# Kernel optimization log

Measured on AMD Instinct MI355X. Metric: run time of the kernel, lower is better.

The kernel has to match this reference:

```python
import jax, jax.numpy as jnp
import numpy as np

B, L, E, H = 8, 1024, 512, 8
E2 = 2 * E
EPS = 1e-5


def _spectral_fc(x, w, fw, fb, n):
    # rfft along feature dim, multiply by rfft of learned filter w (1,n), irfft back, then Linear
    xf = jnp.fft.rfft(x, axis=2, norm='ortho')          # [B,L,n//2+1] complex
    wf = jnp.fft.rfft(w, axis=1, norm='ortho')          # [1,n//2+1] complex
    y = jnp.fft.irfft(xf * wf, n=n, axis=2, norm='ortho')
    return y @ fw + fb


def _layernorm(x, g, b):
    m = jnp.mean(x, axis=-1, keepdims=True)
    v = jnp.mean(jnp.square(x - m), axis=-1, keepdims=True)
    return (x - m) * jax.lax.rsqrt(v + EPS) * g + b


def setup_inputs() -> dict:
    key = jax.random.key(0)
    ks = jax.random.split(key, 32)
    s = 0.02

    def lin_w(k, i, o):
        return (jax.random.normal(k, (i, o), jnp.float32) / np.sqrt(i)).astype(jnp.float32)

    def layer_params(k0, k1, n):
        return (s * jax.random.normal(k0, (1, n), jnp.float32), lin_w(k1, n, n), jnp.zeros((n,), jnp.float32))

    attn_w, attn_fw, attn_fb = layer_params(ks[1], ks[2], E)
    ln0_w, ln0_fw, ln0_fb = layer_params(ks[3], ks[4], E)
    ln1_w, ln1_fw, ln1_fb = layer_params(ks[5], ks[6], E)
    ln2_w, ln2_fw, ln2_fb = layer_params(ks[7], ks[8], E)
    ln3_w, ln3_fw, ln3_fb = layer_params(ks[9], ks[10], E2)
    ln4_w, ln4_fw, ln4_fb = layer_params(ks[11], ks[12], E2)

    return {
        'x': jax.random.normal(ks[0], (B, L, E), jnp.float32),
        'attn_w': attn_w, 'attn_fw': attn_fw, 'attn_fb': attn_fb,
        'ln0_w': ln0_w, 'ln0_fw': ln0_fw, 'ln0_fb': ln0_fb,
        'ln1_w': ln1_w, 'ln1_fw': ln1_fw, 'ln1_fb': ln1_fb,
        'ln2_w': ln2_w, 'ln2_fw': ln2_fw, 'ln2_fb': ln2_fb,
        'ln3_w': ln3_w, 'ln3_fw': ln3_fw, 'ln3_fb': ln3_fb,
        'ln4_w': ln4_w, 'ln4_fw': ln4_fw, 'ln4_fb': ln4_fb,
        'n1_g': jnp.ones((E,), jnp.float32), 'n1_b': jnp.zeros((E,), jnp.float32),
        'n2_g': jnp.ones((E,), jnp.float32), 'n2_b': jnp.zeros((E,), jnp.float32),
    }


def reference(x, attn_w, attn_fw, attn_fb,
              ln0_w, ln0_fw, ln0_fb, ln1_w, ln1_fw, ln1_fb,
              ln2_w, ln2_fw, ln2_fb, ln3_w, ln3_fw, ln3_fb,
              ln4_w, ln4_fw, ln4_fb, n1_g, n1_b, n2_g, n2_b):
    q = _spectral_fc(x, attn_w, attn_fw, attn_fb, E).reshape(B, L, H, E // H)
    scores = jnp.einsum('blhe,bshe->bhls', q, q) * (1.0 / np.sqrt(E))
    A = jax.nn.softmax(scores, axis=-1)
    new_x = jnp.einsum('bhls,bshd->blhd', A, q).reshape(B, L, E)

    x1 = _layernorm(x + new_x, n1_g, n1_b)
    x_ln = jax.nn.gelu(_spectral_fc(x1, ln0_w, ln0_fw, ln0_fb, E), approximate=False)
    x2 = x1 - x_ln
    h = jax.nn.sigmoid(_spectral_fc(x2, ln1_w, ln1_fw, ln1_fb, E)) * _spectral_fc(x2, ln2_w, ln2_fw, ln2_fb, E)
    out = jnp.concatenate((new_x, x_ln), axis=-1)  # [B,L,2E]
    out = jax.nn.sigmoid(_spectral_fc(out, ln3_w, ln3_fw, ln3_fb, E2)) * _spectral_fc(out, ln4_w, ln4_fw, ln4_fb, E2)
    return (_layernorm(h, n2_g, n2_b), out)
```

## Files before the change

### kernel.cpp

```cpp
#include <hip/hip_runtime.h>
#include <hip/hip_bf16.h>
#include <math.h>

typedef __hip_bfloat16 bf16;
typedef unsigned short u16;
typedef __attribute__((ext_vector_type(8))) short short8;
typedef __attribute__((ext_vector_type(4))) float f32x4;

#define NB      8
#define SEQ     1024
#define EDIM    512
#define E2DIM   1024
#define ROWS    8192
#define INV_SQRT_E 0.04419417382415922f
#define ATT_SCL    0.06375985678148161f

__device__ inline u16 f2bu(float f) {
    union { float f; unsigned u; } c; c.f = f;
    return (u16)((c.u + 0x7FFF + ((c.u >> 16) & 1)) >> 16);
}

__device__ __forceinline__ unsigned cvtpk_bf16(float lo, float hi) {
    unsigned r;
    asm("v_cvt_pk_bf16_f32 %0, %1, %2" : "=v"(r) : "v"(lo), "v"(hi));
    return r;
}

#define VMCNT(N) do { \
    asm volatile("s_waitcnt vmcnt(" #N ")" ::: "memory"); \
    __builtin_amdgcn_sched_barrier(0); \
    __builtin_amdgcn_s_barrier(); \
    __builtin_amdgcn_sched_barrier(0); } while (0)

#define LGKM0_BAR() do { \
    asm volatile("s_waitcnt lgkmcnt(0)" ::: "memory"); \
    __builtin_amdgcn_sched_barrier(0); \
    __builtin_amdgcn_s_barrier(); \
    __builtin_amdgcn_sched_barrier(0); } while (0)

__global__ __launch_bounds__(256) void detect_dtype(const u16* __restrict__ x,
                                                    int* __restrict__ flag) {
    int t = threadIdx.x;
    int cnt = 0;
    for (int k = t; k < 8192; k += 256) {
        int e = (x[k] >> 7) & 0xFF;
        if (e >= 0xC0) cnt++;
    }
#pragma unroll
    for (int o = 32; o > 0; o >>= 1) cnt += __shfl_xor(cnt, o);
    __shared__ int red[4];
    if ((t & 63) == 0) red[t >> 6] = cnt;
    __syncthreads();
    if (t == 0) flag[0] = (red[0] + red[1] + red[2] + red[3] > 100) ? 1 : 0;
}

struct CvtBatch {
    const void* src[23];
    float4*     dst[23];
    int         pre4[24];
};

__global__ __launch_bounds__(256) void cvt_all(CvtBatch a, int total4,
                                               const int* __restrict__ flag) {
    int t = blockIdx.x * 256 + threadIdx.x;
    if (t >= total4) return;
    int lo = 0;
    while (t >= a.pre4[lo + 1]) lo++;
    int li = t - a.pre4[lo];
    if (flag[0]) {
        a.dst[lo][li] = ((const float4*)a.src[lo])[li];
    } else {
        ushort4 u = ((const ushort4*)a.src[lo])[li];
        union { unsigned int i; float f; } c;
        float4 o;
        c.i = ((unsigned)u.x) << 16; o.x = c.f;
        c.i = ((unsigned)u.y) << 16; o.y = c.f;
        c.i = ((unsigned)u.z) << 16; o.z = c.f;
        c.i = ((unsigned)u.w) << 16; o.w = c.f;
        a.dst[lo][li] = o;
    }
}

__global__ __launch_bounds__(256) void f2b_kernel(const float* __restrict__ src,
                                                  u16* __restrict__ dst, int n4) {
    int i = blockIdx.x * 256 + threadIdx.x;
    if (i >= n4) return;
    float4 a = ((const float4*)src)[i];
    ushort4 o;
    o.x = f2bu(a.x); o.y = f2bu(a.y); o.z = f2bu(a.z); o.w = f2bu(a.w);
    ((ushort4*)dst)[i] = o;
}

#define LDK 32

__device__ __forceinline__ void stage128x32(const u16* g, int ld, u16* lds, int tid) {
    const int w = tid >> 6;
    const int l = tid & 63;
    const int r = w * 16 + (l >> 2);
    const int c = (l & 3) * 8;
    const u16* g0 = g + (size_t)r * ld + c;
    u16* l0 = lds + w * 16 * LDK;
    __builtin_amdgcn_global_load_lds(
        (const __attribute__((address_space(1))) void*)g0,
        (__attribute__((address_space(3))) void*)l0, 16, 0, 0);
    const u16* g1 = g0 + (size_t)64 * ld;
    u16* l1 = l0 + 64 * LDK;
    __builtin_amdgcn_global_load_lds(
        (const __attribute__((address_space(1))) void*)g1,
        (__attribute__((address_space(3))) void*)l1, 16, 0, 0);
}

__device__ __forceinline__ void stage64x32(const u16* g, int ld, u16* lds, int tid) {
    const int w = tid >> 6;
    const int l = tid & 63;
    const int r = w * 16 + (l >> 2);
    const int c = (l & 3) * 8;
    const u16* g0 = g + (size_t)r * ld + c;
    u16* l0 = lds + w * 16 * LDK;
    __builtin_amdgcn_global_load_lds(
        (const __attribute__((address_space(1))) void*)g0,
        (__attribute__((address_space(3))) void*)l0, 16, 0, 0);
}

__device__ __forceinline__ void xcd_swz(int& bx, int& by) {
    const int nx  = gridDim.x;
    const int nwg = nx * gridDim.y;
    const int lid = blockIdx.y * nx + blockIdx.x;
    const int q   = nwg >> 3;
    const int s   = (lid & 7) * q + (lid >> 3);
    bx = s % nx;
    by = s / nx;
}

struct FoldBatch {
    const float* w[6];
    const float* fw[6];
    u16* t1[6];
    u16* t2[6];
    u16* mt[6];
    int  n[6], lg[6];
    float sc[6];
};

__global__ __launch_bounds__(256) void fold_trconv(FoldBatch fb) {
    const int z = blockIdx.z;
    const int n = fb.n[z];
    const int bx = blockIdx.x * 32, by = blockIdx.y * 32;
    if (bx >= n || by >= n) return;
    __shared__ float t[32][33];
    const int tx = threadIdx.x & 31, ty = threadIdx.x >> 5;
    const float* src = fb.fw[z];
    u16* dst = fb.t1[z];
#pragma unroll
    for (int r = 0; r < 32; r += 8)
        t[ty + r][tx] = src[(size_t)(by + ty + r) * n + bx + tx];
    __syncthreads();
#pragma unroll
    for (int r = 0; r < 32; r += 8)
        dst[(size_t)(bx + ty + r) * n + by + tx] = f2bu(t[tx][ty + r]);
}

__global__ __launch_bounds__(256) void fold_circ(FoldBatch fb) {
    const int z = blockIdx.z;
    const int n = fb.n[z], lg = fb.lg[z];
    int idx = blockIdx.x * 256 + threadIdx.x;
    if (idx >= n * n) return;
    int mask = n - 1;
    int m = idx & mask;
    int j = idx >> lg;
    fb.t2[z][idx] = f2bu(fb.w[z][(m - j) & mask]);
}

__global__ __launch_bounds__(256) void fold_gemm(FoldBatch fb) {
    const int z = blockIdx.z;
    const int n = fb.n[z];
    const int bm = blockIdx.y * 128, bn = blockIdx.x * 128;
    if (bm >= n || bn >= n) return;
    const u16* A  = fb.t1[z];
    const u16* Bt = fb.t2[z];
    u16* Mt = fb.mt[z];
    const float scale = fb.sc[z];

    __shared__ u16 Asl[2][128 * LDK];
    __shared__ u16 Bsl[2][128 * LDK];
    const int tid = threadIdx.x;
    const int lane = tid & 63, wave = tid >> 6;
    const int wy = wave >> 1, wx = wave & 1;
    const int qd = lane >> 4, ln16 = lane & 15;

    f32x4 acc[4][4];
#pragma unroll
    for (int i = 0; i < 4; i++)
#pragma unroll
        for (int j = 0; j < 4; j++)
#pragma unroll
            for (int r = 0; r < 4; r++) acc[i][j][r] = 0.f;

    const u16* Ab = A  + (size_t)bm * n;
    const u16* Bb = Bt + (size_t)bn * n;
    const int nt = n >> 5;
    stage128x32(Ab, n, Asl[0], tid);
    stage128x32(Bb, n, Bsl[0], tid);
    stage128x32(Ab + 32, n, Asl[1], tid);
    stage128x32(Bb + 32, n, Bsl[1], tid);
    int cur = 0;
    for (int t = 0; t < nt - 1; ++t) {
        VMCNT(4);
        const u16* Ac = Asl[cur];
        const u16* Bc = Bsl[cur];
        short8 af[4], bf_[4];
#pragma unroll
        for (int i = 0; i < 4; i++) {
            af[i]  = *(const short8*)&Ac[(wy * 64 + i * 16 + ln16) * LDK + qd * 8];
            bf_[i] = *(const short8*)&Bc[(wx * 64 + i * 16 + ln16) * LDK + qd * 8];
        }
        LGKM0_BAR();
        if (t + 2 < nt) {
            const int k2 = (t + 2) * 32;
            stage128x32(Ab + k2, n, Asl[cur], tid);
            stage128x32(Bb + k2, n, Bsl[cur], tid);
        }
#pragma unroll
        for (int i = 0; i < 4; i++)
#pragma unroll
            for (int j = 0; j < 4; j++)
                acc[i][j] = __builtin_amdgcn_mfma_f32_16x16x32_bf16(af[i], bf_[j], acc[i][j], 0, 0, 0);
        cur ^= 1;
    }
    VMCNT(0);
    {
        const u16* Ac = Asl[cur];
        const u16* Bc = Bsl[cur];
        short8 af[4], bf_[4];
#pragma unroll
        for (int i = 0; i < 4; i++) {
            af[i]  = *(const short8*)&Ac[(wy * 64 + i * 16 + ln16) * LDK + qd * 8];
            bf_[i] = *(const short8*)&Bc[(wx * 64 + i * 16 + ln16) * LDK + qd * 8];
        }
#pragma unroll
        for (int i = 0; i < 4; i++)
#pragma unroll
            for (int j = 0; j < 4; j++)
                acc[i][j] = __builtin_amdgcn_mfma_f32_16x16x32_bf16(af[i], bf_[j], acc[i][j], 0, 0, 0);
    }
#pragma unroll
    for (int i = 0; i < 4; i++)
#pragma unroll
        for (int j = 0; j < 4; j++) {
            const int col = bn + wx * 64 + j * 16 + ln16;
#pragma unroll
            for (int r = 0; r < 4; r++) {
                const int row = bm + wy * 64 + i * 16 + qd * 4 + r;
                Mt[(size_t)row * n + col] = f2bu(acc[i][j][r] * scale);
            }
        }
}

__global__ __launch_bounds__(256) void gemm_bf(
    const u16* __restrict__ A, int lda,
    const u16* __restrict__ Bt, int ldb,
    const float* __restrict__ bias,
    float* __restrict__ Cf, int ldc,
    u16* __restrict__ Cb, int ldcb,
    u16* __restrict__ Cb2, int ldcb2,
    const float* __restrict__ aux, int ldaux,
    int K, int mode)
{
    __shared__ u16 Asl[2][128 * LDK];
    __shared__ u16 Bsl[2][64 * LDK];
    const int tid = threadIdx.x;
    int bxs, bys;
    xcd_swz(bxs, bys);
    const int bm = bys * 128, bn = bxs * 64;
    const int lane = tid & 63, wave = tid >> 6;
    const int wy = wave >> 1, wx = wave & 1;
    const int qd = lane >> 4, ln16 = lane & 15;

    f32x4 acc[4][2];
#pragma unroll
    for (int i = 0; i < 4; i++)
#pragma unroll
        for (int j = 0; j < 2; j++)
#pragma unroll
            for (int r = 0; r < 4; r++) acc[i][j][r] = 0.f;

    const u16* Ab = A  + (size_t)bm * lda;
    const u16* Bb = Bt + (size_t)bn * ldb;
    const int nt = K >> 5;
    stage128x32(Ab, lda, Asl[0], tid);
    stage64x32(Bb, ldb, Bsl[0], tid);
    stage128x32(Ab + 32, lda, Asl[1], tid);
    stage64x32(Bb + 32, ldb, Bsl[1], tid);
    int cur = 0;
    for (int t = 0; t < nt - 1; ++t) {
        VMCNT(3);
        const u16* Ac = Asl[cur];
        const u16* Bc = Bsl[cur];
        short8 af[4], bf_[2];
#pragma unroll
        for (int i = 0; i < 4; i++)
            af[i]  = *(const short8*)&Ac[(wy * 64 + i * 16 + ln16) * LDK + qd * 8];
#pragma unroll
        for (int j = 0; j < 2; j++)
            bf_[j] = *(const short8*)&Bc[(wx * 32 + j * 16 + ln16) * LDK + qd * 8];
        LGKM0_BAR();
        if (t + 2 < nt) {
            const int k2 = (t + 2) * 32;
            stage128x32(Ab + k2, lda, Asl[cur], tid);
            stage64x32(Bb + k2, ldb, Bsl[cur], tid);
        }
#pragma unroll
        for (int i = 0; i < 4; i++)
#pragma unroll
            for (int j = 0; j < 2; j++)
                acc[i][j] = __builtin_amdgcn_mfma_f32_16x16x32_bf16(af[i], bf_[j], acc[i][j], 0, 0, 0);
        cur ^= 1;
    }
    VMCNT(0);
    {
        const u16* Ac = Asl[cur];
        const u16* Bc = Bsl[cur];
        short8 af[4], bf_[2];
#pragma unroll
        for (int i = 0; i < 4; i++)
            af[i]  = *(const short8*)&Ac[(wy * 64 + i * 16 + ln16) * LDK + qd * 8];
#pragma unroll
        for (int j = 0; j < 2; j++)
            bf_[j] = *(const short8*)&Bc[(wx * 32 + j * 16 + ln16) * LDK + qd * 8];
#pragma unroll
        for (int i = 0; i < 4; i++)
#pragma unroll
            for (int j = 0; j < 2; j++)
                acc[i][j] = __builtin_amdgcn_mfma_f32_16x16x32_bf16(af[i], bf_[j], acc[i][j], 0, 0, 0);
    }

#pragma unroll
    for (int i = 0; i < 4; i++) {
#pragma unroll
        for (int j = 0; j < 2; j++) {
            const int col = bn + wx * 32 + j * 16 + ln16;
            const float b_ = bias ? bias[col] : 0.f;
#pragma unroll
            for (int r = 0; r < 4; r++) {
                const int row = bm + wy * 64 + i * 16 + qd * 4 + r;
                float v = acc[i][j][r] + b_;
                if (mode == 1) v = 0.5f * v * (1.0f + erff(v * 0.7071067811865476f));
                if (Cf)  Cf[(size_t)row * ldc + col] = v;
                if (Cb)  Cb[(size_t)row * ldcb + col] = f2bu(v);
                if (Cb2) Cb2[(size_t)row * ldcb2 + col] =
                             f2bu(aux[(size_t)row * ldaux + col] - v);
            }
        }
    }
}

__global__ __launch_bounds__(256) void gemm_bf2(
    const u16* __restrict__ A, int lda,
    const u16* __restrict__ B1t, const u16* __restrict__ B2t, int ldb,
    const float* __restrict__ bias1, const float* __restrict__ bias2,
    float* __restrict__ Cf, int ldc, int K)
{
    __shared__ u16 Asl[2][128 * LDK];
    __shared__ u16 B1sl[2][64 * LDK];
    __shared__ u16 B2sl[2][64 * LDK];
    const int tid = threadIdx.x;
    int bxs, bys;
    xcd_swz(bxs, bys);
    const int bm = bys * 128, bn = bxs * 64;
    const int lane = tid & 63, wave = tid >> 6;
    const int wy = wave >> 1, wx = wave & 1;
    const int qd = lane >> 4, ln16 = lane & 15;

    f32x4 acc1[4][2], acc2[4][2];
#pragma unroll
    for (int i = 0; i < 4; i++)
#pragma unroll
        for (int j = 0; j < 2; j++)
#pragma unroll
            for (int r = 0; r < 4; r++) { acc1[i][j][r] = 0.f; acc2[i][j][r] = 0.f; }

    const u16* Ab  = A   + (size_t)bm * lda;
    const u16* B1b = B1t + (size_t)bn * ldb;
    const u16* B2b = B2t + (size_t)bn * ldb;
    const int nt = K >> 5;
    stage128x32(Ab,  lda, Asl[0],  tid);
    stage64x32(B1b, ldb, B1sl[0], tid);
    stage64x32(B2b, ldb, B2sl[0], tid);
    stage128x32(Ab + 32,  lda, Asl[1],  tid);
    stage64x32(B1b + 32, ldb, B1sl[1], tid);
    stage64x32(B2b + 32, ldb, B2sl[1], tid);
    int cur = 0;
    for (int t = 0; t < nt - 1; ++t) {
        VMCNT(4);
        const u16* Ac  = Asl[cur];
        const u16* B1c = B1sl[cur];
        const u16* B2c = B2sl[cur];
        short8 af[4], b1f[2], b2f[2];
#pragma unroll
        for (int i = 0; i < 4; i++)
            af[i]  = *(const short8*)&Ac [(wy * 64 + i * 16 + ln16) * LDK + qd * 8];
#pragma unroll
        for (int j = 0; j < 2; j++) {
            b1f[j] = *(const short8*)&B1c[(wx * 32 + j * 16 + ln16) * LDK + qd * 8];
            b2f[j] = *(const short8*)&B2c[(wx * 32 + j * 16 + ln16) * LDK + qd * 8];
        }
        LGKM0_BAR();
        if (t + 2 < nt) {
            const int k2 = (t + 2) * 32;
            stage128x32(Ab  + k2, lda, Asl[cur],  tid);
            stage64x32(B1b + k2, ldb, B1sl[cur], tid);
            stage64x32(B2b + k2, ldb, B2sl[cur], tid);
        }
#pragma unroll
        for (int i = 0; i < 4; i++)
#pragma unroll
            for (int j = 0; j < 2; j++) {
                acc1[i][j] = __builtin_amdgcn_mfma_f32_16x16x32_bf16(af[i], b1f[j], acc1[i][j], 0, 0, 0);
                acc2[i][j] = __builtin_amdgcn_mfma_f32_16x16x32_bf16(af[i], b2f[j], acc2[i][j], 0, 0, 0);
            }
        cur ^= 1;
    }
    VMCNT(0);
    {
        const u16* Ac  = Asl[cur];
        const u16* B1c = B1sl[cur];
        const u16* B2c = B2sl[cur];
        short8 af[4], b1f[2], b2f[2];
#pragma unroll
        for (int i = 0; i < 4; i++)
            af[i]  = *(const short8*)&Ac [(wy * 64 + i * 16 + ln16) * LDK + qd * 8];
#pragma unroll
        for (int j = 0; j < 2; j++) {
            b1f[j] = *(const short8*)&B1c[(wx * 32 + j * 16 + ln16) * LDK + qd * 8];
            b2f[j] = *(const short8*)&B2c[(wx * 32 + j * 16 + ln16) * LDK + qd * 8];
        }
#pragma unroll
        for (int i = 0; i < 4; i++)
#pragma unroll
            for (int j = 0; j < 2; j++) {
                acc1[i][j] = __builtin_amdgcn_mfma_f32_16x16x32_bf16(af[i], b1f[j], acc1[i][j], 0, 0, 0);
                acc2[i][j] = __builtin_amdgcn_mfma_f32_16x16x32_bf16(af[i], b2f[j], acc2[i][j], 0, 0, 0);
            }
    }

#pragma unroll
    for (int i = 0; i < 4; i++) {
#pragma unroll
        for (int j = 0; j < 2; j++) {
            const int col = bn + wx * 32 + j * 16 + ln16;
            const float b1_ = bias1[col], b2_ = bias2[col];
#pragma unroll
            for (int r = 0; r < 4; r++) {
                const int row = bm + wy * 64 + i * 16 + qd * 4 + r;
                const float g = 1.0f / (1.0f + expf(-(acc1[i][j][r] + b1_)));
                Cf[(size_t)row * ldc + col] = g * (acc2[i][j][r] + b2_);
            }
        }
    }
}

__global__ __launch_bounds__(256) void ln_kernel(
    const float* __restrict__ in0, int ld0,
    const u16* __restrict__ in1b, int ld1b,
    const float* __restrict__ g, const float* __restrict__ bta,
    float* __restrict__ outf, int ldo,
    u16* __restrict__ outb, int ldob)
{
    int row = blockIdx.x, tid = threadIdx.x;
    const float* p0 = in0 + (size_t)row * ld0;
    float v0 = p0[tid], v1 = p0[tid + 256];
    if (in1b) {
        const u16* p1 = in1b + (size_t)row * ld1b;
        union { unsigned u; float f; } c0, c1;
        c0.u = ((unsigned)p1[tid]) << 16;
        c1.u = ((unsigned)p1[tid + 256]) << 16;
        v0 += c0.f; v1 += c1.f;
    }
    float s = v0 + v1, sq = v0 * v0 + v1 * v1;
#pragma unroll
    for (int o = 32; o > 0; o >>= 1) {
        s  += __shfl_xor(s, o);
        sq += __shfl_xor(sq, o);
    }
    __shared__ float red[8];
    int wid = tid >> 6;
    if ((tid & 63) == 0) { red[wid] = s; red[4 + wid] = sq; }
    __syncthreads();
    s  = red[0] + red[1] + red[2] + red[3];
    sq = red[4] + red[5] + red[6] + red[7];
    float mean = s * (1.0f / 512.0f);
    float var  = sq * (1.0f / 512.0f) - mean * mean;
    float rstd = rsqrtf(var + 1e-5f);
    float o0 = (v0 - mean) * rstd * g[tid] + bta[tid];
    float o1 = (v1 - mean) * rstd * g[tid + 256] + bta[tid + 256];
    if (outf) {
        outf[(size_t)row * ldo + tid]       = o0;
        outf[(size_t)row * ldo + tid + 256] = o1;
    }
    if (outb) {
        outb[(size_t)row * ldob + tid]       = f2bu(o0);
        outb[(size_t)row * ldob + tid + 256] = f2bu(o1);
    }
}

#define AP 80

__global__ __launch_bounds__(256) void attn_mfma(const u16* __restrict__ qall,
                                                 u16* __restrict__ catb) {
    __shared__ u16 Ks[64 * AP];
    __shared__ u16 KsT[64 * AP];
    __shared__ u16 Pw[4][16 * AP];

    const int bid = blockIdx.x;
    const int lt = bid & 15, hh = (bid >> 4) & 7, bb = bid >> 7;
    const int q0 = lt * 64;
    const int tid = threadIdx.x;
    const int wave = tid >> 6, lane = tid & 63;
    const int quad = lane >> 4, ln16 = lane & 15;

    const u16* qh = qall + (size_t)bb * SEQ * EDIM + hh * 64;

    const u16* qrow = qh + (size_t)(q0 + wave * 16 + ln16) * EDIM + quad * 8;
    const short8 aq0 = *(const short8*)(qrow);
    const short8 aq1 = *(const short8*)(qrow + 32);

    f32x4 oacc[4];
    float m_run = -1e30f, l_run = 0.f;
#pragma unroll
    for (int j = 0; j < 4; j++)
#pragma unroll
        for (int r = 0; r < 4; r++) oacc[j][r] = 0.f;

    const int sr  = tid & 63;
    const int scq = (tid >> 6) * 16;

    for (int s0 = 0; s0 < SEQ; s0 += 64) {
        __syncthreads();
        {
            const u16* krow = qh + (size_t)(s0 + sr) * EDIM + scq;
            uint4 v0 = *(const uint4*)(krow);
            uint4 v1 = *(const uint4*)(krow + 8);
            *(uint4*)&Ks[sr * AP + scq]     = v0;
            *(uint4*)&Ks[sr * AP + scq + 8] = v1;
            const u16* h0 = (const u16*)&v0;
            const u16* h1 = (const u16*)&v1;
#pragma unroll
            for (int i = 0; i < 8; i++) KsT[(scq + i) * AP + sr]     = h0[i];
#pragma unroll
            for (int i = 0; i < 8; i++) KsT[(scq + 8 + i) * AP + sr] = h1[i];
        }
        __syncthreads();

        f32x4 S[4];
#pragma unroll
        for (int j = 0; j < 4; j++) {
            const int krw = (j * 16 + ln16) * AP + quad * 8;
            short8 a0 = *(const short8*)&Ks[krw];
            short8 a1 = *(const short8*)&Ks[krw + 32];
            f32x4 c = {0.f, 0.f, 0.f, 0.f};
            c = __builtin_amdgcn_mfma_f32_16x16x32_bf16(a0, aq0, c, 0, 0, 0);
            c = __builtin_amdgcn_mfma_f32_16x16x32_bf16(a1, aq1, c, 0, 0, 0);
            S[j] = c;
        }

        float mx = S[0][0];
#pragma unroll
        for (int j = 0; j < 4; j++)
#pragma unroll
            for (int r = 0; r < 4; r++) mx = fmaxf(mx, S[j][r]);
        mx = fmaxf(mx, __shfl_xor(mx, 16));
        mx = fmaxf(mx, __shfl_xor(mx, 32));
        const float mn = fmaxf(m_run, mx);
        const float al = exp2f((m_run - mn) * ATT_SCL);
        m_run = mn;
        const float ns = -mn * ATT_SCL;
        float p[4][4];
        float rs = 0.f;
#pragma unroll
        for (int j = 0; j < 4; j++)
#pragma unroll
            for (int r = 0; r < 4; r++) {
                p[j][r] = exp2f(fmaf(S[j][r], ATT_SCL, ns));
                rs += p[j][r];
            }
        rs += __shfl_xor(rs, 16);
        rs += __shfl_xor(rs, 32);
        l_run = l_run * al + rs;

#pragma unroll
        for (int j = 0; j < 4; j++) {
            unsigned w0 = cvtpk_bf16(p[j][0], p[j][1]);
            unsigned w1 = cvtpk_bf16(p[j][2], p[j][3]);
            *(uint2*)&Pw[wave][ln16 * AP + j * 16 + quad * 4] = make_uint2(w0, w1);
        }

        float alq[4];
#pragma unroll
        for (int r = 0; r < 4; r++) alq[r] = __shfl(al, quad * 4 + r);
#pragma unroll
        for (int j = 0; j < 4; j++)
#pragma unroll
            for (int r = 0; r < 4; r++) oacc[j][r] *= alq[r];

        short8 pa0 = *(const short8*)&Pw[wave][ln16 * AP + quad * 8];
        short8 pa1 = *(const short8*)&Pw[wave][ln16 * AP + 32 + quad * 8];

#pragma unroll
        for (int j = 0; j < 4; j++) {
            const int drw = (j * 16 + ln16) * AP + quad * 8;
            short8 b0 = *(const short8*)&KsT[drw];
            short8 b1 = *(const short8*)&KsT[drw + 32];
            oacc[j] = __builtin_amdgcn_mfma_f32_16x16x32_bf16(pa0, b0, oacc[j], 0, 0, 0);
            oacc[j] = __builtin_amdgcn_mfma_f32_16x16x32_bf16(pa1, b1, oacc[j], 0, 0, 0);
        }
    }

    const float linv = 1.0f / l_run;
    float invq[4];
#pragma unroll
    for (int r = 0; r < 4; r++) invq[r] = __shfl(linv, quad * 4 + r);
#pragma unroll
    for (int r = 0; r < 4; r++) {
        const int row = bb * SEQ + q0 + wave * 16 + quad * 4 + r;
#pragma unroll
        for (int j = 0; j < 4; j++) {
            const int col = hh * 64 + j * 16 + ln16;
            catb[(size_t)row * E2DIM + col] = f2bu(oacc[j][r] * invq[r]);
        }
    }
}

extern "C" void kernel_launch(void* const* d_in, const int* in_sizes, int n_in,
                              void* d_out, int out_size, void* d_ws, size_t ws_size,
                              hipStream_t stream)
{
    const size_t OFF_MT0 = 0;
    const size_t OFF_MT1 = OFF_MT0 + 131072;
    const size_t OFF_MT2 = OFF_MT1 + 131072;
    const size_t OFF_MT3 = OFF_MT2 + 131072;
    const size_t OFF_MT4 = OFF_MT3 + 131072;
    const size_t OFF_MT5 = OFF_MT4 + 524288;
    const size_t OFF_XB  = OFF_MT5 + 524288;
    const size_t OFF_CB  = OFF_XB + 2097152;
    const size_t OFF_BQ  = OFF_CB + 4194304;
    const size_t OFF_BN  = OFF_BQ + 4194304;
    const size_t OFF_BC  = OFF_BN + 4194304;
    const size_t OFF_P   = OFF_BC + 4194304;

    float* W = (float*)d_ws;
    u16* MT[6] = {(u16*)(W + OFF_MT0), (u16*)(W + OFF_MT1), (u16*)(W + OFF_MT2),
                  (u16*)(W + OFF_MT3), (u16*)(W + OFF_MT4), (u16*)(W + OFF_MT5)};
    u16*   XB  = (u16*)(W + OFF_XB);
    u16*   CB  = (u16*)(W + OFF_CB);
    u16*   QB  = (u16*)(W + OFF_BQ);
    float* BN  = W + OFF_BN;
    float* BC  = W + OFF_BC;

    float* F[23];
    CvtBatch cb;
    int pre = 0;
    for (int i = 0; i < 23 && i < n_in; i++) {
        cb.pre4[i] = pre;
        F[i] = W + OFF_P + (size_t)pre * 4;
        cb.src[i] = d_in[i];
        cb.dst[i] = (float4*)F[i];
        pre += in_sizes[i] / 4;
    }
    cb.pre4[23] = pre;
    const int total4 = pre;
    int* FLAG = (int*)(W + OFF_P + (size_t)total4 * 4);

    if (n_in < 23) return;
    if (ws_size < (OFF_P + (size_t)total4 * 4 + 16) * sizeof(float)) return;

    detect_dtype<<<1, 256, 0, stream>>>((const u16*)d_in[0], FLAG);
    cvt_all<<<(total4 + 255) / 256, 256, 0, stream>>>(cb, total4, FLAG);
    f2b_kernel<<<(ROWS * EDIM / 4 + 255) / 256, 256, 0, stream>>>(F[0], XB, ROWS * EDIM / 4);

    FoldBatch fb;
    {
        const int wi[6] = {1, 4, 7, 10, 13, 16};
        u16* T1 = (u16*)BN;
        u16* T2 = (u16*)BC;
        size_t off = 0;
        for (int s = 0; s < 6; s++) {
            const int n = (s < 4) ? 512 : 1024;
            fb.w[s]  = F[wi[s]];
            fb.fw[s] = F[wi[s] + 1];
            fb.t1[s] = T1 + off;
            fb.t2[s] = T2 + off;
            fb.mt[s] = MT[s];
            fb.n[s]  = n;
            fb.lg[s] = (s < 4) ? 9 : 10;
            fb.sc[s] = (s < 4) ? 0.04419417382415922f : 0.03125f;
            off += (size_t)n * n;
        }
    }
    fold_trconv<<<dim3(32, 32, 6), 256, 0, stream>>>(fb);
    fold_circ<<<dim3(4096, 1, 6), 256, 0, stream>>>(fb);
    fold_gemm<<<dim3(8, 8, 6), 256, 0, stream>>>(fb);

    float* out0 = (float*)d_out;
    float* out1 = (float*)d_out + (size_t)ROWS * EDIM;

    gemm_bf<<<dim3(8, 64), 256, 0, stream>>>(
        XB, 512, MT[0], 512, F[3], nullptr, 0, QB, 512, nullptr, 0, nullptr, 0, 512, 0);
    attn_mfma<<<1024, 256, 0, stream>>>(QB, CB);
    ln_kernel<<<8192, 256, 0, stream>>>(F[0], 512, CB, 1024, F[19], F[20],
                                        BC, 512, XB, 512);
    gemm_bf<<<dim3(8, 64), 256, 0, stream>>>(
        XB, 512, MT[1], 512, F[6], nullptr, 0, CB + 512, 1024, QB, 512, BC, 512, 512, 1);
    gemm_bf2<<<dim3(8, 64), 256, 0, stream>>>(
        QB, 512, MT[2], MT[3], 512, F[9], F[12], BN, 512, 512);
    ln_kernel<<<8192, 256, 0, stream>>>(BN, 512, nullptr, 0, F[21], F[22],
                                        out0, 512, nullptr, 0);
    gemm_bf2<<<dim3(16, 64), 256, 0, stream>>>(
        CB, 1024, MT[4], MT[5], 1024, F[15], F[18], out1, 1024, 1024);
}
```

Measured before the change: 334.4 us.

## Pre-transpose V and double-buffer attention K/V tiles via async LDS loads

Adds a separate kernel that writes a transposed copy of Q (used as V) per batch and head into a reused scratch buffer. The attention kernel then stages K and V^T tiles with global_load_lds into XOR-swizzled, double-buffered LDS and prefetches two tiles ahead, replacing the per-iteration synchronous load and scalar LDS transpose. The intent is to overlap global loads with MFMA work and to remove the costly element-wise transposed LDS stores and bank conflicts. In exchange it adds one kernel launch and the extra traffic of writing and reading the transposed copy, and it relies on the vmcnt/lgkm wait macros for correctness because there are no __syncthreads left in the loop.

```diff
diff --git a/kernel.cpp b/kernel.cpp
--- a/kernel.cpp
+++ b/kernel.cpp
@@ -120,6 +120,20 @@
     __builtin_amdgcn_global_load_lds(
         (const __attribute__((address_space(1))) void*)g0,
         (__attribute__((address_space(3))) void*)l0, 16, 0, 0);
+}
+
+__device__ __forceinline__ void stage64x64sw(const u16* g0, int ld, u16* lds,
+                                             int wave, int lane) {
+#pragma unroll
+    for (int c = 0; c < 2; c++) {
+        const int r  = wave * 16 + c * 8 + (lane >> 3);
+        const int cg = (lane & 7) ^ (r & 7);
+        const u16* g = g0 + (size_t)r * ld + cg * 8;
+        u16* l = lds + (wave * 16 + c * 8) * 64;
+        __builtin_amdgcn_global_load_lds(
+            (const __attribute__((address_space(1))) void*)g,
+            (__attribute__((address_space(3))) void*)l, 16, 0, 0);
+    }
 }
 
 __device__ __forceinline__ void xcd_swz(int& bx, int& by) {
@@ -503,12 +517,34 @@
     }
 }
 
+__global__ __launch_bounds__(256) void trans_vt(const u16* __restrict__ q,
+                                                u16* __restrict__ vt) {
+    const int z  = blockIdx.z;
+    const int bb = z >> 3, hh = z & 7;
+    const int k0 = blockIdx.x * 64;
+    const int d0 = blockIdx.y * 32;
+    __shared__ u16 t[64][33];
+    const int tx = threadIdx.x & 31, ty = threadIdx.x >> 5;
+    const u16* src = q + (size_t)(bb * SEQ + k0) * EDIM + hh * 64 + d0;
+#pragma unroll
+    for (int r = 0; r < 64; r += 8)
+        t[ty + r][tx] = src[(size_t)(ty + r) * EDIM + tx];
+    __syncthreads();
+    const int ox = threadIdx.x & 63, oy = threadIdx.x >> 6;
+    u16* dst = vt + ((size_t)z * 64 + d0) * SEQ + k0;
+#pragma unroll
+    for (int r = 0; r < 32; r += 4)
+        dst[(size_t)(oy + r) * SEQ + ox] = t[ox][oy + r];
+}
+
 #define AP 80
+#define ANT 16
 
 __global__ __launch_bounds__(256) void attn_mfma(const u16* __restrict__ qall,
+                                                 const u16* __restrict__ vt,
                                                  u16* __restrict__ catb) {
-    __shared__ u16 Ks[64 * AP];
-    __shared__ u16 KsT[64 * AP];
+    __shared__ u16 Ks2[2][64 * 64];
+    __shared__ u16 VTs2[2][64 * 64];
     __shared__ u16 Pw[4][16 * AP];
 
     const int bid = blockIdx.x;
@@ -519,6 +555,7 @@
     const int quad = lane >> 4, ln16 = lane & 15;
 
     const u16* qh = qall + (size_t)bb * SEQ * EDIM + hh * 64;
+    const u16* vh = vt + (size_t)(bb * 8 + hh) * 64 * SEQ;
 
     const u16* qrow = qh + (size_t)(q0 + wave * 16 + ln16) * EDIM + quad * 8;
     const short8 aq0 = *(const short8*)(qrow);
@@ -531,32 +568,27 @@
 #pragma unroll
         for (int r = 0; r < 4; r++) oacc[j][r] = 0.f;
 
-    const int sr  = tid & 63;
-    const int scq = (tid >> 6) * 16;
-
-    for (int s0 = 0; s0 < SEQ; s0 += 64) {
-        __syncthreads();
-        {
-            const u16* krow = qh + (size_t)(s0 + sr) * EDIM + scq;
-            uint4 v0 = *(const uint4*)(krow);
-            uint4 v1 = *(const uint4*)(krow + 8);
-            *(uint4*)&Ks[sr * AP + scq]     = v0;
-            *(uint4*)&Ks[sr * AP + scq + 8] = v1;
-            const u16* h0 = (const u16*)&v0;
-            const u16* h1 = (const u16*)&v1;
-#pragma unroll
-            for (int i = 0; i < 8; i++) KsT[(scq + i) * AP + sr]     = h0[i];
-#pragma unroll
-            for (int i = 0; i < 8; i++) KsT[(scq + 8 + i) * AP + sr] = h1[i];
-        }
-        __syncthreads();
+    stage64x64sw(qh, EDIM, Ks2[0], wave, lane);
+    stage64x64sw(vh, SEQ, VTs2[0], wave, lane);
+    stage64x64sw(qh + (size_t)64 * EDIM, EDIM, Ks2[1], wave, lane);
+    stage64x64sw(vh + 64, SEQ, VTs2[1], wave, lane);
+
+    const int sw = ln16 & 7;
+    const int c0 = (quad ^ sw) * 8;
+    const int c1 = ((quad + 4) ^ sw) * 8;
+
+    int cur = 0;
+    for (int t = 0; t < ANT; ++t) {
+        if (t < ANT - 1) { VMCNT(4); } else { VMCNT(0); }
+        const u16* Kc = Ks2[cur];
+        const u16* Vc = VTs2[cur];
 
         f32x4 S[4];
 #pragma unroll
         for (int j = 0; j < 4; j++) {
-            const int krw = (j * 16 + ln16) * AP + quad * 8;
-            short8 a0 = *(const short8*)&Ks[krw];
-            short8 a1 = *(const short8*)&Ks[krw + 32];
+            const int ro = (j * 16 + ln16) * 64;
+            short8 a0 = *(const short8*)&Kc[ro + c0];
+            short8 a1 = *(const short8*)&Kc[ro + c1];
             f32x4 c = {0.f, 0.f, 0.f, 0.f};
             c = __builtin_amdgcn_mfma_f32_16x16x32_bf16(a0, aq0, c, 0, 0, 0);
             c = __builtin_amdgcn_mfma_f32_16x16x32_bf16(a1, aq1, c, 0, 0, 0);
@@ -604,15 +636,26 @@
 
         short8 pa0 = *(const short8*)&Pw[wave][ln16 * AP + quad * 8];
         short8 pa1 = *(const short8*)&Pw[wave][ln16 * AP + 32 + quad * 8];
-
+        short8 vb0[4], vb1[4];
 #pragma unroll
         for (int j = 0; j < 4; j++) {
-            const int drw = (j * 16 + ln16) * AP + quad * 8;
-            short8 b0 = *(const short8*)&KsT[drw];
-            short8 b1 = *(const short8*)&KsT[drw + 32];
-            oacc[j] = __builtin_amdgcn_mfma_f32_16x16x32_bf16(pa0, b0, oacc[j], 0, 0, 0);
-            oacc[j] = __builtin_amdgcn_mfma_f32_16x16x32_bf16(pa1, b1, oacc[j], 0, 0, 0);
-        }
+            const int ro = (j * 16 + ln16) * 64;
+            vb0[j] = *(const short8*)&Vc[ro + c0];
+            vb1[j] = *(const short8*)&Vc[ro + c1];
+        }
+
+        LGKM0_BAR();
+        if (t + 2 < ANT) {
+            stage64x64sw(qh + (size_t)(t + 2) * 64 * EDIM, EDIM, Ks2[cur], wave, lane);
+            stage64x64sw(vh + (t + 2) * 64, SEQ, VTs2[cur], wave, lane);
+        }
+
+#pragma unroll
+        for (int j = 0; j < 4; j++) {
+            oacc[j] = __builtin_amdgcn_mfma_f32_16x16x32_bf16(pa0, vb0[j], oacc[j], 0, 0, 0);
+            oacc[j] = __builtin_amdgcn_mfma_f32_16x16x32_bf16(pa1, vb1[j], oacc[j], 0, 0, 0);
+        }
+        cur ^= 1;
     }
 
     const float linv = 1.0f / l_run;
@@ -655,6 +698,7 @@
     u16*   QB  = (u16*)(W + OFF_BQ);
     float* BN  = W + OFF_BN;
     float* BC  = W + OFF_BC;
+    u16*   VT  = (u16*)BN;
 
     float* F[23];
     CvtBatch cb;
@@ -705,7 +749,8 @@
 
     gemm_bf<<<dim3(8, 64), 256, 0, stream>>>(
         XB, 512, MT[0], 512, F[3], nullptr, 0, QB, 512, nullptr, 0, nullptr, 0, 512, 0);
-    attn_mfma<<<1024, 256, 0, stream>>>(QB, CB);
+    trans_vt<<<dim3(16, 2, 64), 256, 0, stream>>>(QB, VT);
+    attn_mfma<<<1024, 256, 0, stream>>>(QB, VT, CB);
     ln_kernel<<<8192, 256, 0, stream>>>(F[0], 512, CB, 1024, F[19], F[20],
                                         BC, 512, XB, 512);
     gemm_bf<<<dim3(8, 64), 256, 0, stream>>>(
```

New measurement: 347.1 us. 1.04x slower.
